# Optimization experiments

Hardware: AMD Instinct MI355X
Metric: run time of the kernel (lower is better)

The kernel has to match this reference:

```python
import jax, jax.numpy as jnp
import numpy as np

D_MODEL, N_HEAD, D_HEAD = 1024, 16, 64
QLEN, MLEN, BSZ = 1024, 512, 4
KLEN = QLEN + MLEN
RLEN = QLEN + KLEN
SCALE = 1.0 / (D_HEAD ** 0.5)
LN_EPS = 1e-12


def rel_shift(x, klen):
    # x: [i, j, b, n] -> shifted [i, klen, b, n]
    i, j, b, n = x.shape
    x = x.reshape(j, i, b, n)[1:].reshape(i, j - 1, b, n)
    return x[:, :klen]


def layer_norm(x, gamma, beta, eps=LN_EPS):
    mu = jnp.mean(x, axis=-1, keepdims=True)
    var = jnp.mean(jnp.square(x - mu), axis=-1, keepdims=True)
    return (x - mu) * jax.lax.rsqrt(var + eps) * gamma + beta


def setup_inputs() -> dict:
    key = jax.random.key(0)
    ks = jax.random.split(key, 16)
    std = 0.02
    h = jax.random.normal(ks[0], (QLEN, BSZ, D_MODEL), jnp.float32)
    r = jax.random.normal(ks[1], (RLEN, BSZ, D_MODEL), jnp.float32)
    mems = jax.random.normal(ks[2], (MLEN, BSZ, D_MODEL), jnp.float32)
    # binary float mask (1 = masked), broadcast over head dim
    attn_mask = (jax.random.uniform(ks[3], (QLEN, KLEN, BSZ, 1)) < 0.1).astype(jnp.float32)
    # one-hot segment matrix over 2 segment classes
    seg_ids = jax.random.randint(ks[4], (QLEN, KLEN, BSZ), 0, 2)
    seg_mat = jax.nn.one_hot(seg_ids, 2, dtype=jnp.float32)
    Wq = std * jax.random.normal(ks[5], (D_MODEL, N_HEAD, D_HEAD), jnp.float32)
    Wk = std * jax.random.normal(ks[6], (D_MODEL, N_HEAD, D_HEAD), jnp.float32)
    Wv = std * jax.random.normal(ks[7], (D_MODEL, N_HEAD, D_HEAD), jnp.float32)
    Wo = std * jax.random.normal(ks[8], (D_MODEL, N_HEAD, D_HEAD), jnp.float32)
    Wr = std * jax.random.normal(ks[9], (D_MODEL, N_HEAD, D_HEAD), jnp.float32)
    r_w_bias = jnp.zeros((N_HEAD, D_HEAD), jnp.float32)
    r_r_bias = jnp.zeros((N_HEAD, D_HEAD), jnp.float32)
    r_s_bias = jnp.zeros((N_HEAD, D_HEAD), jnp.float32)
    seg_embed = std * jax.random.normal(ks[10], (2, N_HEAD, D_HEAD), jnp.float32)
    ln_gamma = jnp.ones((D_MODEL,), jnp.float32)
    ln_beta = jnp.zeros((D_MODEL,), jnp.float32)
    return dict(h=h, r=r, mems=mems, attn_mask=attn_mask, seg_mat=seg_mat,
                Wq=Wq, Wk=Wk, Wv=Wv, Wo=Wo, Wr=Wr,
                r_w_bias=r_w_bias, r_r_bias=r_r_bias, r_s_bias=r_s_bias,
                seg_embed=seg_embed, ln_gamma=ln_gamma, ln_beta=ln_beta)


def reference(h, r, mems, attn_mask, seg_mat, Wq, Wk, Wv, Wo, Wr,
              r_w_bias, r_r_bias, r_s_bias, seg_embed, ln_gamma, ln_beta):
    cat = jnp.concatenate([mems, h], axis=0)  # [klen, b, d_model]
    q_head = jnp.einsum('ibh,hnd->ibnd', h, Wq)
    k_head_h = jnp.einsum('jbh,hnd->jbnd', cat, Wk)
    v_head_h = jnp.einsum('jbh,hnd->jbnd', cat, Wv)
    k_head_r = jnp.einsum('jbh,hnd->jbnd', r, Wr)

    klen = k_head_h.shape[0]
    ac = jnp.einsum('ibnd,jbnd->ijbn', q_head + r_w_bias, k_head_h)
    bd = jnp.einsum('ibnd,jbnd->ijbn', q_head + r_r_bias, k_head_r)
    bd = rel_shift(bd, klen)
    ef = jnp.einsum('ibnd,snd->ibns', q_head + r_s_bias, seg_embed)
    ef = jnp.einsum('ijbs,ibns->ijbn', seg_mat, ef)

    attn_score = (ac + bd + ef) * SCALE - 1e30 * attn_mask
    attn_prob = jax.nn.softmax(attn_score, axis=1)
    attn_vec = jnp.einsum('ijbn,jbnd->ibnd', attn_prob, v_head_h)

    attn_out = jnp.einsum('ibnd,hnd->ibh', attn_vec, Wo) + h  # residual
    return layer_norm(attn_out, ln_gamma, ln_beta)
```

## Files before the change

### kernel.cpp

```cpp
#include <hip/hip_runtime.h>

typedef unsigned short u16;
typedef __attribute__((ext_vector_type(8))) short bf16x8;
typedef __attribute__((ext_vector_type(4))) float f32x4;

constexpr int DM = 1024;
constexpr int NH = 16;
constexpr int DH = 64;
constexpr int QL = 1024;
constexpr int ML = 512;
constexpr int KL = 1536;
constexpr int RL = 2560;
constexpr int BS = 4;
constexpr int JT = KL / 64;
constexpr float SCALE = 0.125f;
constexpr float SC2 = 0.125f * 1.4426950408889634f;

static __device__ __forceinline__ u16 f2bf(float f) {
    unsigned u = __float_as_uint(f);
    u += 0x7fffu + ((u >> 16) & 1u);
    return (u16)(u >> 16);
}

static __device__ __forceinline__ void glds16(const u16* g, u16* l) {
    __builtin_amdgcn_global_load_lds(
        (const __attribute__((address_space(1))) unsigned int*)g,
        (__attribute__((address_space(3))) unsigned int*)l,
        16, 0, 0);
}

__global__ __launch_bounds__(256) void prep_kernel(
    const float* __restrict__ mems, const float* __restrict__ h,
    const float* __restrict__ r, const float* __restrict__ Wo,
    const float* __restrict__ mask, const float* __restrict__ segm,
    const float* __restrict__ Wq, const float* __restrict__ Wk,
    const float* __restrict__ Wv, const float* __restrict__ Wr,
    u16* __restrict__ catb, u16* __restrict__ rb, u16* __restrict__ wob,
    u16* __restrict__ WqT, u16* __restrict__ WkT,
    u16* __restrict__ WvT, u16* __restrict__ WrT,
    ulonglong2* __restrict__ pk)
{
    __shared__ float smem[64 * 65];
    const int id = blockIdx.x;
    const int t = threadIdx.x;

    if (id < 17408) {
        const long C0 = (long)ML * BS * DM;
        const long C1 = (long)KL * BS * DM;
        const long C2 = C1 + (long)RL * BS * DM;
        long g = ((long)id * 256 + t) * 4;
        const float* src; u16* dst;
        if (g < C0)      { src = mems + g;        dst = catb + g; }
        else if (g < C1) { src = h + (g - C0);    dst = catb + g; }
        else if (g < C2) { src = r + (g - C1);    dst = rb + (g - C1); }
        else             { src = Wo + (g - C2);   dst = wob + (g - C2); }
        float4 v = *(const float4*)src;
        unsigned lo = (unsigned)f2bf(v.x) | ((unsigned)f2bf(v.y) << 16);
        unsigned hi = (unsigned)f2bf(v.z) | ((unsigned)f2bf(v.w) << 16);
        *(uint2*)dst = make_uint2(lo, hi);
        return;
    }
    if (id < 18432) {
        float (*tile)[65] = (float(*)[65])smem;
        const int local = id - 17408;
        const float* W; u16* WT;
        switch (local >> 8) {
            case 0:  W = Wq; WT = WqT; break;
            case 1:  W = Wk; WT = WkT; break;
            case 2:  W = Wv; WT = WvT; break;
            default: W = Wr; WT = WrT; break;
        }
        const int k0 = (local & 15) * 64, n0 = ((local >> 4) & 15) * 64;
        const int tr = t >> 6, tc = t & 63;
        #pragma unroll
        for (int rr = 0; rr < 16; rr++) {
            int rw = tr + rr * 4;
            tile[rw][tc] = W[(size_t)(k0 + rw) * DM + n0 + tc];
        }
        __syncthreads();
        #pragma unroll
        for (int rr = 0; rr < 16; rr++) {
            int n = tr + rr * 4;
            WT[(size_t)(n0 + n) * DM + k0 + tc] = f2bf(tile[tc][n]);
        }
        return;
    }
    {
        float* mk = smem;
        float* sg = smem + 256;
        const int local = id - 18432;
        const int i = local / JT, jt = local - i * JT;
        const size_t base = ((size_t)i * KL + jt * 64) * BS;
        mk[t] = mask[base + t];
        float2 s2 = ((const float2*)(segm + base * 2))[t];
        sg[t] = s2.y;
        __syncthreads();
        const int b = t >> 6, lane = t & 63;
        const unsigned long long mb = __ballot(mk[lane * 4 + b] > 0.5f);
        const unsigned long long sb = __ballot(sg[lane * 4 + b] > 0.5f);
        if (lane == 0) {
            ulonglong2 v; v.x = mb; v.y = sb;
            pk[(((size_t)b * 16 + (i >> 6)) * JT + jt) * 64 + (i & 63)] = v;
        }
    }
}

__global__ __launch_bounds__(256) void proj_kernel(
    const u16* __restrict__ hb, const u16* __restrict__ catb,
    const u16* __restrict__ rb,
    const u16* __restrict__ WqT, const u16* __restrict__ WkT,
    const u16* __restrict__ WvT, const u16* __restrict__ WrT,
    float* __restrict__ q_s, u16* __restrict__ k_s,
    u16* __restrict__ v_s, u16* __restrict__ kr_s)
{
    __shared__ u16 a_lds[128][32];
    __shared__ u16 b_lds[128][32];
    const int id = blockIdx.x;
    const u16 *A, *B; void* C; int SEQ, MODE, local;
    if (id < 256)       { A = hb;   B = WqT; C = q_s;  SEQ = QL; MODE = 1; local = id; }
    else if (id < 640)  { A = catb; B = WkT; C = k_s;  SEQ = KL; MODE = 2; local = id - 256; }
    else if (id < 1024) { A = catb; B = WvT; C = v_s;  SEQ = KL; MODE = 2; local = id - 640; }
    else                { A = rb;   B = WrT; C = kr_s; SEQ = RL; MODE = 2; local = id - 1024; }
    const int bm = local >> 3, bnn = local & 7;

    const int t = threadIdx.x;
    const int w = t >> 6, lane = t & 63, l15 = lane & 15, q4 = lane >> 4;
    const int wm = (w >> 1) * 64, wn = (w & 1) * 64;
    const int srow = w * 32 + (lane >> 2);
    const int scol = (lane & 3) * 8;
    const u16* Ab = A + (size_t)(bm * 128 + srow) * DM + scol;
    const u16* Bb = B + (size_t)(bnn * 128 + srow) * DM + scol;
    u16* a_dst = &a_lds[w * 32][0];
    u16* b_dst = &b_lds[w * 32][0];

    f32x4 acc[4][4] = {};

    for (int k0 = 0; k0 < DM; k0 += 32) {
        __syncthreads();
        glds16(Ab + k0,           a_dst);
        glds16(Ab + k0 + 16 * DM, a_dst + 16 * 32);
        glds16(Bb + k0,           b_dst);
        glds16(Bb + k0 + 16 * DM, b_dst + 16 * 32);
        __syncthreads();
        bf16x8 af[4], bf[4];
        #pragma unroll
        for (int rt = 0; rt < 4; rt++)
            af[rt] = *(const bf16x8*)&a_lds[wm + rt * 16 + l15][q4 * 8];
        #pragma unroll
        for (int ct = 0; ct < 4; ct++)
            bf[ct] = *(const bf16x8*)&b_lds[wn + ct * 16 + l15][q4 * 8];
        #pragma unroll
        for (int rt = 0; rt < 4; rt++)
            #pragma unroll
            for (int ct = 0; ct < 4; ct++)
                acc[rt][ct] = __builtin_amdgcn_mfma_f32_16x16x32_bf16(
                    af[rt], bf[ct], acc[rt][ct], 0, 0, 0);
    }

    #pragma unroll
    for (int rt = 0; rt < 4; rt++)
      #pragma unroll
      for (int ct = 0; ct < 4; ct++)
        #pragma unroll
        for (int rg = 0; rg < 4; rg++) {
            const int R = bm * 128 + wm + rt * 16 + q4 * 4 + rg;
            const int Cc = bnn * 128 + wn + ct * 16 + l15;
            const float v = acc[rt][ct][rg];
            const int sq = R >> 2, bb = R & 3, hn = Cc >> 6, dd = Cc & 63;
            const size_t idx = ((size_t)(bb * NH + hn) * SEQ + sq) * DH + dd;
            if (MODE == 1) ((float*)C)[idx] = v;
            else           ((u16*)C)[idx]  = f2bf(v);
        }
}

__global__ __launch_bounds__(256) void vtrans_kernel(
    const u16* __restrict__ v_s, u16* __restrict__ vt_s)
{
    __shared__ u16 tl[64][72];
    const int j0 = blockIdx.x * 64;
    const int bn = blockIdx.y;
    const u16* vin = v_s + (size_t)bn * KL * DH;
    u16* vout = vt_s + (size_t)bn * DH * KL;
    const int t = threadIdx.x;
    const int r = t >> 3, c8 = (t & 7) * 8;
    #pragma unroll
    for (int it = 0; it < 64; it += 32)
        *(uint4*)&tl[r + it][c8] = *(const uint4*)(vin + (size_t)(j0 + r + it) * DH + c8);
    __syncthreads();
    #pragma unroll
    for (int it = 0; it < 64; it += 32) {
        const int d = r + it;
        u16 tmp[8];
        #pragma unroll
        for (int jj = 0; jj < 8; jj++) tmp[jj] = tl[c8 + jj][d];
        *(uint4*)&vout[(size_t)d * KL + j0 + c8] = *(const uint4*)tmp;
    }
}

__global__ __launch_bounds__(256) void ogemm_kernel(
    const u16* __restrict__ A, const u16* __restrict__ B,
    float* __restrict__ Cout)
{
    __shared__ u16 a_lds[128][32];
    __shared__ u16 b_lds[128][32];
    const int bm = blockIdx.x, bnn = blockIdx.y;
    const int t = threadIdx.x;
    const int w = t >> 6, lane = t & 63, l15 = lane & 15, q4 = lane >> 4;
    const int wm = (w >> 1) * 64, wn = (w & 1) * 64;
    const int srow = w * 32 + (lane >> 2);
    const int scol = (lane & 3) * 8;
    const u16* Ab = A + (size_t)(bm * 128 + srow) * DM + scol;
    const u16* Bb = B + (size_t)(bnn * 128 + srow) * DM + scol;
    u16* a_dst = &a_lds[w * 32][0];
    u16* b_dst = &b_lds[w * 32][0];

    f32x4 acc[4][4] = {};

    for (int k0 = 0; k0 < DM; k0 += 32) {
        __syncthreads();
        glds16(Ab + k0,           a_dst);
        glds16(Ab + k0 + 16 * DM, a_dst + 16 * 32);
        glds16(Bb + k0,           b_dst);
        glds16(Bb + k0 + 16 * DM, b_dst + 16 * 32);
        __syncthreads();
        bf16x8 af[4], bf[4];
        #pragma unroll
        for (int rt = 0; rt < 4; rt++)
            af[rt] = *(const bf16x8*)&a_lds[wm + rt * 16 + l15][q4 * 8];
        #pragma unroll
        for (int ct = 0; ct < 4; ct++)
            bf[ct] = *(const bf16x8*)&b_lds[wn + ct * 16 + l15][q4 * 8];
        #pragma unroll
        for (int rt = 0; rt < 4; rt++)
            #pragma unroll
            for (int ct = 0; ct < 4; ct++)
                acc[rt][ct] = __builtin_amdgcn_mfma_f32_16x16x32_bf16(
                    af[rt], bf[ct], acc[rt][ct], 0, 0, 0);
    }

    #pragma unroll
    for (int rt = 0; rt < 4; rt++)
      #pragma unroll
      for (int ct = 0; ct < 4; ct++)
        #pragma unroll
        for (int rg = 0; rg < 4; rg++) {
            const int R = bm * 128 + wm + rt * 16 + q4 * 4 + rg;
            const int C = bnn * 128 + wn + ct * 16 + l15;
            Cout[(size_t)R * DM + C] = acc[rt][ct][rg];
        }
}

#define FBAR() do { asm volatile("" ::: "memory");  \
                    __builtin_amdgcn_s_barrier();   \
                    asm volatile("" ::: "memory"); } while (0)

#define STAGE_K(TI)                                                            \
  {                                                                            \
    glds16(kg + (size_t)(TI) * 64 * DH,      &k2[(TI) & 1][0][w * 16][0]);     \
    glds16(kg + (size_t)(TI) * 64 * DH + 32, &k2[(TI) & 1][1][w * 16][0]);     \
  }

#define STAGE_V(TI)                                                            \
  {                                                                            \
    glds16(vg + (TI) * 64,      &v2[(TI) & 1][0][w * 16][0]);                  \
    glds16(vg + (TI) * 64 + 32, &v2[(TI) & 1][1][w * 16][0]);                  \
  }

#define STAGE_PK(TI)                                                           \
    glds16((const u16*)(pk_b + ((size_t)(TI) * 64 + lane)),                    \
           (u16*)&pk_lds[(TI) & 1][0]);

#define STAGE_KR(P)                                                            \
  {                                                                            \
    const int br_ = QL - i0 - 63 + (P) * 64 + w * 16 + krow;                   \
    glds16(kr_bn + (size_t)br_ * DH + ksrcseg * 8,       &krp[(P) & 3][w * 16][0]);     \
    glds16(kr_bn + (size_t)(br_ + 8) * DH + ksrcseg * 8, &krp[(P) & 3][w * 16 + 8][0]); \
  }

__global__ __launch_bounds__(256, 2) void attn_kernel(
    const float* __restrict__ q_s, const u16* __restrict__ k_s,
    const u16* __restrict__ vt_s, const u16* __restrict__ kr_s,
    const ulonglong2* __restrict__ pk,
    const float* __restrict__ rwb, const float* __restrict__ rrb,
    const float* __restrict__ rsb, const float* __restrict__ seg_embed,
    u16* __restrict__ av_s)
{
    __shared__ u16 k2[2][2][64][32];
    __shared__ u16 v2[2][2][64][32];
    __shared__ u16 krp[4][64][64];
    __shared__ u16 p_lds[4][16][64];
    __shared__ ulonglong2 pk_lds[2][64];
    __shared__ float e_lds[2][64];

    const int bn = blockIdx.x;
    const int itile = blockIdx.y;
    const int b = bn >> 4, n = bn & 15;
    const int t = threadIdx.x;
    const int w = t >> 6, lane = t & 63, l15 = lane & 15, q4 = lane >> 4;
    const int i0 = itile * 64;
    const int ib = i0 + w * 16;

    const float* q_bn = q_s + (size_t)bn * QL * DH;
    const u16* k_bn   = k_s  + (size_t)bn * KL * DH;
    const u16* vt_bn  = vt_s + (size_t)bn * DH * KL;
    const u16* kr_bn  = kr_s + (size_t)bn * RL * DH;
    const ulonglong2* pk_b = pk + ((size_t)b * 16 + itile) * JT * 64;

    if (t < 128) {
        const int rr = t >> 1, s = t & 1;
        const float* qrow = q_bn + (size_t)(i0 + rr) * DH;
        const float* se = seg_embed + (s * NH + n) * DH;
        const float* bias = rsb + n * DH;
        float acc = 0.f;
        #pragma unroll 16
        for (int d = 0; d < DH; d++) acc += (qrow[d] + bias[d]) * se[d];
        e_lds[s][rr] = acc * SC2;
    }

    bf16x8 qw[2], qr[2];
    {
        const float* qrow = q_bn + (size_t)(ib + l15) * DH;
        const float* bw = rwb + n * DH;
        const float* br = rrb + n * DH;
        #pragma unroll
        for (int kk = 0; kk < 2; kk++) {
            const int dbase = kk * 32 + q4 * 8;
            #pragma unroll
            for (int j = 0; j < 8; j++) {
                float qv = qrow[dbase + j];
                qw[kk][j] = (short)f2bf((qv + bw[dbase + j]) * SC2);
                qr[kk][j] = (short)f2bf((qv + br[dbase + j]) * SC2);
            }
        }
    }

    const int srow = lane >> 2;
    const int ssw  = ((lane & 3) ^ ((srow >> 1) & 3)) * 8;
    const u16* kg = k_bn  + (size_t)(w * 16 + srow) * DH + ssw;
    const u16* vg = vt_bn + (size_t)(w * 16 + srow) * KL + ssw;

    const int krow = lane >> 3;
    const int ksrcseg = (lane & 7) ^ krow;

    const int sA = ((q4)     ^ (l15 & 7)) * 8;
    const int sB = ((q4 + 4) ^ (l15 & 7)) * 8;
    const int ksw = (l15 >> 1) & 3;
    const int lrb_p = 48 - w * 16;

    f32x4 o[4] = {};
    float l_r[4] = {0.f, 0.f, 0.f, 0.f};

    STAGE_K(0); STAGE_V(0); STAGE_PK(0);
    STAGE_KR(0); STAGE_KR(1);
    STAGE_K(1); STAGE_V(1); STAGE_PK(1);
    STAGE_KR(2);
    asm volatile("s_waitcnt vmcnt(7) lgkmcnt(0)" ::: "memory");
    FBAR();

    float e_rg[2][4];
    #pragma unroll
    for (int rg = 0; rg < 4; rg++) {
        e_rg[0][rg] = e_lds[0][w * 16 + q4 * 4 + rg];
        e_rg[1][rg] = e_lds[1][w * 16 + q4 * 4 + rg];
    }

    #pragma unroll 1
    for (int jt = 0; jt < JT; jt++) {
        const int cb = jt & 1;

        __builtin_amdgcn_s_setprio(1);
        f32x4 sac[4] = {};
        #pragma unroll
        for (int ct = 0; ct < 4; ct++) {
            bf16x8 kb0 = *(const bf16x8*)&k2[cb][0][ct * 16 + l15][(q4 ^ ksw) * 8];
            bf16x8 kb1 = *(const bf16x8*)&k2[cb][1][ct * 16 + l15][(q4 ^ ksw) * 8];
            sac[ct] = __builtin_amdgcn_mfma_f32_16x16x32_bf16(qw[0], kb0, sac[ct], 0, 0, 0);
            sac[ct] = __builtin_amdgcn_mfma_f32_16x16x32_bf16(qw[1], kb1, sac[ct], 0, 0, 0);
        }

        f32x4 bacc[5] = {};
        #pragma unroll
        for (int wc = 0; wc < 5; wc++) {
            const int S = lrb_p + wc * 16;
            const u16* pr_ = &krp[(jt + (S >> 6)) & 3][(S & 63) + l15][0];
            bf16x8 b0 = *(const bf16x8*)(pr_ + sA);
            bf16x8 b1 = *(const bf16x8*)(pr_ + sB);
            bacc[wc] = __builtin_amdgcn_mfma_f32_16x16x32_bf16(qr[0], b0, bacc[wc], 0, 0, 0);
            bacc[wc] = __builtin_amdgcn_mfma_f32_16x16x32_bf16(qr[1], b1, bacc[wc], 0, 0, 0);
        }
        __builtin_amdgcn_s_setprio(0);

        #pragma unroll
        for (int rg = 0; rg < 4; rg++) {
            const int row = q4 * 4 + rg;
            const ulonglong2 mp = pk_lds[cb][w * 16 + row];
            const unsigned long long mx = mp.x >> l15;
            const unsigned long long sy = mp.y >> l15;
            const int v = l15 + 15 - row;
            const int srcl = (q4 << 4) | (v & 15);
            float sh[5];
            #pragma unroll
            for (int w5 = 0; w5 < 5; w5++)
                sh[w5] = __shfl(bacc[w5][rg], srcl, 64);
            const float e0 = e_rg[0][rg];
            const float e1 = e_rg[1][rg];
            float s0 = 0.f;
            #pragma unroll
            for (int ct = 0; ct < 4; ct++) {
                const float bd = (v < 16) ? sh[ct] : sh[ct + 1];
                const float ef = ((sy >> (ct * 16)) & 1ull) ? e1 : e0;
                float sarg = sac[ct][rg] + bd + ef;
                sarg = ((mx >> (ct * 16)) & 1ull) ? -1.0e30f : sarg;
                const float p = __builtin_amdgcn_exp2f(sarg);
                const int pg = (2 * ct + (l15 >> 3)) ^ (row & 7);
                p_lds[w][row][pg * 8 + (l15 & 7)] = f2bf(p);
                s0 += p;
            }
            l_r[rg] += s0;
        }

        __builtin_amdgcn_s_setprio(1);
        #pragma unroll
        for (int kk = 0; kk < 2; kk++) {
            const int pgr = ((kk * 4 + q4) ^ (l15 & 7)) * 8;
            bf16x8 pf = *(const bf16x8*)&p_lds[w][l15][pgr];
            #pragma unroll
            for (int dt = 0; dt < 4; dt++) {
                bf16x8 vf = *(const bf16x8*)&v2[cb][kk][dt * 16 + l15][(q4 ^ ksw) * 8];
                o[dt] = __builtin_amdgcn_mfma_f32_16x16x32_bf16(pf, vf, o[dt], 0, 0, 0);
            }
        }
        __builtin_amdgcn_s_setprio(0);

        if (jt < JT - 1) {
            FBAR();
            if (jt + 2 < JT) {
                STAGE_K(jt + 2);
                STAGE_V(jt + 2);
                STAGE_PK(jt + 2);
                STAGE_KR(jt + 3);
                asm volatile("s_waitcnt vmcnt(7)" ::: "memory");
            } else {
                asm volatile("s_waitcnt vmcnt(0)" ::: "memory");
            }
            FBAR();
        }
    }

    #pragma unroll
    for (int rg = 0; rg < 4; rg++) {
        #pragma unroll
        for (int off = 1; off < 16; off <<= 1)
            l_r[rg] += __shfl_xor(l_r[rg], off, 64);
        l_r[rg] = 1.f / l_r[rg];
    }
    #pragma unroll
    for (int dt = 0; dt < 4; dt++)
        #pragma unroll
        for (int rg = 0; rg < 4; rg++) {
            const int row = q4 * 4 + rg;
            const int ii = ib + row;
            const int d = dt * 16 + l15;
            const float v = o[dt][rg] * l_r[rg];
            av_s[(size_t)(ii * BS + b) * DM + n * DH + d] = f2bf(v);
        }
}

__global__ __launch_bounds__(256) void ln_kernel(
    const float* __restrict__ ao, const float* __restrict__ h,
    const float* __restrict__ gamma, const float* __restrict__ beta,
    float* __restrict__ out)
{
    __shared__ float red[8];
    const int row = blockIdx.x, t = threadIdx.x;
    const float* a  = ao + (size_t)row * DM;
    const float* hh = h  + (size_t)row * DM;
    float4 av = *(const float4*)(a + t * 4);
    float4 hv = *(const float4*)(hh + t * 4);
    const float x0 = av.x + hv.x, x1 = av.y + hv.y;
    const float x2 = av.z + hv.z, x3 = av.w + hv.w;
    float s = x0 + x1 + x2 + x3;
    float s2 = x0 * x0 + x1 * x1 + x2 * x2 + x3 * x3;
    #pragma unroll
    for (int off = 1; off < 64; off <<= 1) {
        s  += __shfl_xor(s, off, 64);
        s2 += __shfl_xor(s2, off, 64);
    }
    const int w = t >> 6;
    if ((t & 63) == 0) { red[w] = s; red[4 + w] = s2; }
    __syncthreads();
    s  = red[0] + red[1] + red[2] + red[3];
    s2 = red[4] + red[5] + red[6] + red[7];
    const float mu = s * (1.f / DM);
    const float var = s2 * (1.f / DM) - mu * mu;
    const float rstd = rsqrtf(var + 1e-12f);
    float4 g  = *(const float4*)(gamma + t * 4);
    float4 bb = *(const float4*)(beta + t * 4);
    float4 ov;
    ov.x = (x0 - mu) * rstd * g.x + bb.x;
    ov.y = (x1 - mu) * rstd * g.y + bb.y;
    ov.z = (x2 - mu) * rstd * g.z + bb.z;
    ov.w = (x3 - mu) * rstd * g.w + bb.w;
    *(float4*)(out + (size_t)row * DM + t * 4) = ov;
}

extern "C" void kernel_launch(void* const* d_in, const int* in_sizes, int n_in,
                              void* d_out, int out_size, void* d_ws, size_t ws_size,
                              hipStream_t stream) {
    (void)in_sizes; (void)n_in; (void)out_size; (void)ws_size;
    const float* h    = (const float*)d_in[0];
    const float* r    = (const float*)d_in[1];
    const float* mems = (const float*)d_in[2];
    const float* mask = (const float*)d_in[3];
    const float* segm = (const float*)d_in[4];
    const float* Wq   = (const float*)d_in[5];
    const float* Wk   = (const float*)d_in[6];
    const float* Wv   = (const float*)d_in[7];
    const float* Wo   = (const float*)d_in[8];
    const float* Wr   = (const float*)d_in[9];
    const float* rwb  = (const float*)d_in[10];
    const float* rrb  = (const float*)d_in[11];
    const float* rsb  = (const float*)d_in[12];
    const float* semb = (const float*)d_in[13];
    const float* gam  = (const float*)d_in[14];
    const float* bet  = (const float*)d_in[15];
    float* out = (float*)d_out;

    char* wsb = (char*)d_ws;
    size_t off = 0;
    auto alloc = [&](size_t bytes) -> void* {
        void* p = wsb + off; off += (bytes + 255) & ~(size_t)255; return p;
    };
    u16* catb = (u16*)alloc((size_t)KL * BS * DM * 2);
    u16* rb   = (u16*)alloc((size_t)RL * BS * DM * 2);
    u16* WqT  = (u16*)alloc((size_t)DM * DM * 2);
    u16* WkT  = (u16*)alloc((size_t)DM * DM * 2);
    u16* WvT  = (u16*)alloc((size_t)DM * DM * 2);
    u16* WrT  = (u16*)alloc((size_t)DM * DM * 2);
    u16* WoB  = (u16*)alloc((size_t)DM * DM * 2);
    float* q_s = (float*)alloc((size_t)BS * NH * QL * DH * 4);
    u16* k_s  = (u16*)alloc((size_t)BS * NH * KL * DH * 2);
    u16* vt_s = (u16*)alloc((size_t)BS * NH * KL * DH * 2);
    u16* kr_s = (u16*)alloc((size_t)BS * NH * RL * DH * 2 + 8192);
    u16* av_s = (u16*)alloc((size_t)QL * BS * DM * 2);
    float* ao_s = (float*)alloc((size_t)QL * BS * DM * 4);
    ulonglong2* pk = (ulonglong2*)alloc((size_t)BS * QL * JT * 16);
    u16* v_s = (u16*)ao_s;

    prep_kernel<<<43008, 256, 0, stream>>>(mems, h, r, Wo, mask, segm,
                                           Wq, Wk, Wv, Wr,
                                           catb, rb, WoB,
                                           WqT, WkT, WvT, WrT, pk);
    const u16* hb = catb + (size_t)2048 * DM;
    proj_kernel<<<1664, 256, 0, stream>>>(hb, catb, rb, WqT, WkT, WvT, WrT,
                                          q_s, k_s, v_s, kr_s);
    vtrans_kernel<<<dim3(JT, 64), 256, 0, stream>>>(v_s, vt_s);
    attn_kernel<<<dim3(64, 16), 256, 0, stream>>>(q_s, k_s, vt_s, kr_s, pk,
                                                  rwb, rrb, rsb, semb, av_s);
    ogemm_kernel<<<dim3(32, 8), 256, 0, stream>>>(av_s, WoB, ao_s);
    ln_kernel<<<4096, 256, 0, stream>>>(ao_s, h, gam, bet, out);
}
```

Baseline: 514.8 us.

## Double attention query tile to 128 rows and single-buffer V staging

Each attention block now handles 128 query rows instead of 64, with each wave owning two 16-row groups. Each K and V tile loaded into LDS is therefore reused across twice as many MFMAs, and the grid halves to 512 blocks. The packed mask/segment layout changes to match 128-row tiles. V staging drops to a single buffer loaded one iteration ahead and the KR prefetch moves to a mid-iteration barrier, which adds a barrier per loop, raises register pressure and cuts the number of blocks, possibly lowering occupancy on the CUs.

```diff
diff --git a/kernel.cpp b/kernel.cpp
--- a/kernel.cpp
+++ b/kernel.cpp
@@ -100,7 +100,7 @@
         const unsigned long long sb = __ballot(sg[lane * 4 + b] > 0.5f);
         if (lane == 0) {
             ulonglong2 v; v.x = mb; v.y = sb;
-            pk[(((size_t)b * 16 + (i >> 6)) * JT + jt) * 64 + (i & 63)] = v;
+            pk[(((size_t)b * 8 + (i >> 7)) * JT + jt) * 128 + (i & 127)] = v;
         }
     }
 }
@@ -262,17 +262,21 @@
 
 #define STAGE_V(TI)                                                            \
   {                                                                            \
-    glds16(vg + (TI) * 64,      &v2[(TI) & 1][0][w * 16][0]);                  \
-    glds16(vg + (TI) * 64 + 32, &v2[(TI) & 1][1][w * 16][0]);                  \
+    glds16(vg + (TI) * 64,      &v1[0][w * 16][0]);                            \
+    glds16(vg + (TI) * 64 + 32, &v1[1][w * 16][0]);                            \
   }
 
 #define STAGE_PK(TI)                                                           \
-    glds16((const u16*)(pk_b + ((size_t)(TI) * 64 + lane)),                    \
-           (u16*)&pk_lds[(TI) & 1][0]);
+  {                                                                            \
+    glds16((const u16*)(pk_b + ((size_t)(TI) * 128 + lane)),                   \
+           (u16*)&pk_lds[(TI) & 1][0]);                                        \
+    glds16((const u16*)(pk_b + ((size_t)(TI) * 128 + 64 + lane)),              \
+           (u16*)&pk_lds[(TI) & 1][64]);                                       \
+  }
 
 #define STAGE_KR(P)                                                            \
   {                                                                            \
-    const int br_ = QL - i0 - 63 + (P) * 64 + w * 16 + krow;                   \
+    const int br_ = PbaseG + (P) * 64 + w * 16 + krow;                         \
     glds16(kr_bn + (size_t)br_ * DH + ksrcseg * 8,       &krp[(P) & 3][w * 16][0]);     \
     glds16(kr_bn + (size_t)(br_ + 8) * DH + ksrcseg * 8, &krp[(P) & 3][w * 16 + 8][0]); \
   }
@@ -286,27 +290,28 @@
     u16* __restrict__ av_s)
 {
     __shared__ u16 k2[2][2][64][32];
-    __shared__ u16 v2[2][2][64][32];
+    __shared__ u16 v1[2][64][32];
     __shared__ u16 krp[4][64][64];
-    __shared__ u16 p_lds[4][16][64];
-    __shared__ ulonglong2 pk_lds[2][64];
-    __shared__ float e_lds[2][64];
+    __shared__ u16 p_lds[4][32][64];
+    __shared__ ulonglong2 pk_lds[2][128];
+    __shared__ float e_lds[2][128];
 
     const int bn = blockIdx.x;
     const int itile = blockIdx.y;
     const int b = bn >> 4, n = bn & 15;
     const int t = threadIdx.x;
     const int w = t >> 6, lane = t & 63, l15 = lane & 15, q4 = lane >> 4;
-    const int i0 = itile * 64;
-    const int ib = i0 + w * 16;
+    const int i0 = itile * 128;
+    const int ib = i0 + w * 32;
+    const int PbaseG = QL - i0 - 127;
 
     const float* q_bn = q_s + (size_t)bn * QL * DH;
     const u16* k_bn   = k_s  + (size_t)bn * KL * DH;
     const u16* vt_bn  = vt_s + (size_t)bn * DH * KL;
     const u16* kr_bn  = kr_s + (size_t)bn * RL * DH;
-    const ulonglong2* pk_b = pk + ((size_t)b * 16 + itile) * JT * 64;
-
-    if (t < 128) {
+    const ulonglong2* pk_b = pk + ((size_t)b * 8 + itile) * (JT * 128);
+
+    {
         const int rr = t >> 1, s = t & 1;
         const float* qrow = q_bn + (size_t)(i0 + rr) * DH;
         const float* se = seg_embed + (s * NH + n) * DH;
@@ -317,9 +322,10 @@
         e_lds[s][rr] = acc * SC2;
     }
 
-    bf16x8 qw[2], qr[2];
-    {
-        const float* qrow = q_bn + (size_t)(ib + l15) * DH;
+    bf16x8 qw[2][2], qr[2][2];
+    #pragma unroll
+    for (int g = 0; g < 2; g++) {
+        const float* qrow = q_bn + (size_t)(ib + g * 16 + l15) * DH;
         const float* bw = rwb + n * DH;
         const float* br = rrb + n * DH;
         #pragma unroll
@@ -328,8 +334,8 @@
             #pragma unroll
             for (int j = 0; j < 8; j++) {
                 float qv = qrow[dbase + j];
-                qw[kk][j] = (short)f2bf((qv + bw[dbase + j]) * SC2);
-                qr[kk][j] = (short)f2bf((qv + br[dbase + j]) * SC2);
+                qw[g][kk][j] = (short)f2bf((qv + bw[dbase + j]) * SC2);
+                qr[g][kk][j] = (short)f2bf((qv + br[dbase + j]) * SC2);
             }
         }
     }
@@ -345,125 +351,146 @@
     const int sA = ((q4)     ^ (l15 & 7)) * 8;
     const int sB = ((q4 + 4) ^ (l15 & 7)) * 8;
     const int ksw = (l15 >> 1) & 3;
-    const int lrb_p = 48 - w * 16;
-
-    f32x4 o[4] = {};
-    float l_r[4] = {0.f, 0.f, 0.f, 0.f};
-
-    STAGE_K(0); STAGE_V(0); STAGE_PK(0);
-    STAGE_KR(0); STAGE_KR(1);
-    STAGE_K(1); STAGE_V(1); STAGE_PK(1);
-    STAGE_KR(2);
-    asm volatile("s_waitcnt vmcnt(7) lgkmcnt(0)" ::: "memory");
+
+    f32x4 o[2][4] = {};
+    float l_r[2][4] = {};
+
+    STAGE_K(0); STAGE_PK(0);
+    STAGE_KR(0); STAGE_KR(1); STAGE_KR(2);
+    STAGE_V(0); STAGE_K(1); STAGE_PK(1);
+    asm volatile("s_waitcnt vmcnt(6) lgkmcnt(0)" ::: "memory");
     FBAR();
 
-    float e_rg[2][4];
-    #pragma unroll
-    for (int rg = 0; rg < 4; rg++) {
-        e_rg[0][rg] = e_lds[0][w * 16 + q4 * 4 + rg];
-        e_rg[1][rg] = e_lds[1][w * 16 + q4 * 4 + rg];
-    }
+    float e_rg[2][2][4];
+    #pragma unroll
+    for (int g = 0; g < 2; g++)
+        #pragma unroll
+        for (int rg = 0; rg < 4; rg++) {
+            e_rg[0][g][rg] = e_lds[0][w * 32 + g * 16 + q4 * 4 + rg];
+            e_rg[1][g][rg] = e_lds[1][w * 32 + g * 16 + q4 * 4 + rg];
+        }
 
     #pragma unroll 1
     for (int jt = 0; jt < JT; jt++) {
         const int cb = jt & 1;
 
         __builtin_amdgcn_s_setprio(1);
-        f32x4 sac[4] = {};
+        f32x4 sac[2][4] = {};
         #pragma unroll
         for (int ct = 0; ct < 4; ct++) {
             bf16x8 kb0 = *(const bf16x8*)&k2[cb][0][ct * 16 + l15][(q4 ^ ksw) * 8];
             bf16x8 kb1 = *(const bf16x8*)&k2[cb][1][ct * 16 + l15][(q4 ^ ksw) * 8];
-            sac[ct] = __builtin_amdgcn_mfma_f32_16x16x32_bf16(qw[0], kb0, sac[ct], 0, 0, 0);
-            sac[ct] = __builtin_amdgcn_mfma_f32_16x16x32_bf16(qw[1], kb1, sac[ct], 0, 0, 0);
-        }
-
-        f32x4 bacc[5] = {};
-        #pragma unroll
-        for (int wc = 0; wc < 5; wc++) {
-            const int S = lrb_p + wc * 16;
-            const u16* pr_ = &krp[(jt + (S >> 6)) & 3][(S & 63) + l15][0];
-            bf16x8 b0 = *(const bf16x8*)(pr_ + sA);
-            bf16x8 b1 = *(const bf16x8*)(pr_ + sB);
-            bacc[wc] = __builtin_amdgcn_mfma_f32_16x16x32_bf16(qr[0], b0, bacc[wc], 0, 0, 0);
-            bacc[wc] = __builtin_amdgcn_mfma_f32_16x16x32_bf16(qr[1], b1, bacc[wc], 0, 0, 0);
+            sac[0][ct] = __builtin_amdgcn_mfma_f32_16x16x32_bf16(qw[0][0], kb0, sac[0][ct], 0, 0, 0);
+            sac[0][ct] = __builtin_amdgcn_mfma_f32_16x16x32_bf16(qw[0][1], kb1, sac[0][ct], 0, 0, 0);
+            sac[1][ct] = __builtin_amdgcn_mfma_f32_16x16x32_bf16(qw[1][0], kb0, sac[1][ct], 0, 0, 0);
+            sac[1][ct] = __builtin_amdgcn_mfma_f32_16x16x32_bf16(qw[1][1], kb1, sac[1][ct], 0, 0, 0);
         }
         __builtin_amdgcn_s_setprio(0);
 
         #pragma unroll
-        for (int rg = 0; rg < 4; rg++) {
-            const int row = q4 * 4 + rg;
-            const ulonglong2 mp = pk_lds[cb][w * 16 + row];
-            const unsigned long long mx = mp.x >> l15;
-            const unsigned long long sy = mp.y >> l15;
-            const int v = l15 + 15 - row;
-            const int srcl = (q4 << 4) | (v & 15);
-            float sh[5];
-            #pragma unroll
-            for (int w5 = 0; w5 < 5; w5++)
-                sh[w5] = __shfl(bacc[w5][rg], srcl, 64);
-            const float e0 = e_rg[0][rg];
-            const float e1 = e_rg[1][rg];
-            float s0 = 0.f;
-            #pragma unroll
-            for (int ct = 0; ct < 4; ct++) {
-                const float bd = (v < 16) ? sh[ct] : sh[ct + 1];
-                const float ef = ((sy >> (ct * 16)) & 1ull) ? e1 : e0;
-                float sarg = sac[ct][rg] + bd + ef;
-                sarg = ((mx >> (ct * 16)) & 1ull) ? -1.0e30f : sarg;
-                const float p = __builtin_amdgcn_exp2f(sarg);
-                const int pg = (2 * ct + (l15 >> 3)) ^ (row & 7);
-                p_lds[w][row][pg * 8 + (l15 & 7)] = f2bf(p);
-                s0 += p;
+        for (int g = 0; g < 2; g++) {
+            const int bg = 112 - w * 32 - g * 16;
+            __builtin_amdgcn_s_setprio(1);
+            f32x4 bacc[5] = {};
+            #pragma unroll
+            for (int wc = 0; wc < 5; wc++) {
+                const int S = bg + wc * 16;
+                const u16* pr_ = &krp[(jt + (S >> 6)) & 3][(S & 63) + l15][0];
+                bf16x8 b0 = *(const bf16x8*)(pr_ + sA);
+                bf16x8 b1 = *(const bf16x8*)(pr_ + sB);
+                bacc[wc] = __builtin_amdgcn_mfma_f32_16x16x32_bf16(qr[g][0], b0, bacc[wc], 0, 0, 0);
+                bacc[wc] = __builtin_amdgcn_mfma_f32_16x16x32_bf16(qr[g][1], b1, bacc[wc], 0, 0, 0);
             }
-            l_r[rg] += s0;
-        }
+            __builtin_amdgcn_s_setprio(0);
+
+            #pragma unroll
+            for (int rg = 0; rg < 4; rg++) {
+                const int row = q4 * 4 + rg;
+                const ulonglong2 mp = pk_lds[cb][w * 32 + g * 16 + row];
+                const unsigned long long mx = mp.x >> l15;
+                const unsigned long long sy = mp.y >> l15;
+                const int v = l15 + 15 - row;
+                const int srcl = (q4 << 4) | (v & 15);
+                float sh[5];
+                #pragma unroll
+                for (int w5 = 0; w5 < 5; w5++)
+                    sh[w5] = __shfl(bacc[w5][rg], srcl, 64);
+                const float e0 = e_rg[0][g][rg];
+                const float e1 = e_rg[1][g][rg];
+                float s0 = 0.f;
+                #pragma unroll
+                for (int ct = 0; ct < 4; ct++) {
+                    const float bd = (v < 16) ? sh[ct] : sh[ct + 1];
+                    const float ef = ((sy >> (ct * 16)) & 1ull) ? e1 : e0;
+                    float sarg = sac[g][ct][rg] + bd + ef;
+                    sarg = ((mx >> (ct * 16)) & 1ull) ? -1.0e30f : sarg;
+                    const float p = __builtin_amdgcn_exp2f(sarg);
+                    const int pg = (2 * ct + (l15 >> 3)) ^ (row & 7);
+                    p_lds[w][g * 16 + row][pg * 8 + (l15 & 7)] = f2bf(p);
+                    s0 += p;
+                }
+                l_r[g][rg] += s0;
+            }
+        }
+
+        if (jt == JT - 1) asm volatile("s_waitcnt vmcnt(0)" ::: "memory");
+        else              asm volatile("s_waitcnt vmcnt(4)" ::: "memory");
+        FBAR();
+        if (jt < JT - 1) STAGE_KR(jt + 3);
 
         __builtin_amdgcn_s_setprio(1);
         #pragma unroll
         for (int kk = 0; kk < 2; kk++) {
-            const int pgr = ((kk * 4 + q4) ^ (l15 & 7)) * 8;
-            bf16x8 pf = *(const bf16x8*)&p_lds[w][l15][pgr];
-            #pragma unroll
-            for (int dt = 0; dt < 4; dt++) {
-                bf16x8 vf = *(const bf16x8*)&v2[cb][kk][dt * 16 + l15][(q4 ^ ksw) * 8];
-                o[dt] = __builtin_amdgcn_mfma_f32_16x16x32_bf16(pf, vf, o[dt], 0, 0, 0);
+            bf16x8 vf[4];
+            #pragma unroll
+            for (int dt = 0; dt < 4; dt++)
+                vf[dt] = *(const bf16x8*)&v1[kk][dt * 16 + l15][(q4 ^ ksw) * 8];
+            #pragma unroll
+            for (int g = 0; g < 2; g++) {
+                const int pgr = ((kk * 4 + q4) ^ (l15 & 7)) * 8;
+                bf16x8 pf = *(const bf16x8*)&p_lds[w][g * 16 + l15][pgr];
+                #pragma unroll
+                for (int dt = 0; dt < 4; dt++)
+                    o[g][dt] = __builtin_amdgcn_mfma_f32_16x16x32_bf16(pf, vf[dt], o[g][dt], 0, 0, 0);
             }
         }
         __builtin_amdgcn_s_setprio(0);
 
         if (jt < JT - 1) {
             FBAR();
+            STAGE_V(jt + 1);
             if (jt + 2 < JT) {
                 STAGE_K(jt + 2);
-                STAGE_V(jt + 2);
                 STAGE_PK(jt + 2);
-                STAGE_KR(jt + 3);
-                asm volatile("s_waitcnt vmcnt(7)" ::: "memory");
+                asm volatile("s_waitcnt vmcnt(6)" ::: "memory");
             } else {
-                asm volatile("s_waitcnt vmcnt(0)" ::: "memory");
+                asm volatile("s_waitcnt vmcnt(2)" ::: "memory");
             }
             FBAR();
         }
     }
 
     #pragma unroll
-    for (int rg = 0; rg < 4; rg++) {
-        #pragma unroll
-        for (int off = 1; off < 16; off <<= 1)
-            l_r[rg] += __shfl_xor(l_r[rg], off, 64);
-        l_r[rg] = 1.f / l_r[rg];
-    }
-    #pragma unroll
-    for (int dt = 0; dt < 4; dt++)
+    for (int g = 0; g < 2; g++)
         #pragma unroll
         for (int rg = 0; rg < 4; rg++) {
-            const int row = q4 * 4 + rg;
-            const int ii = ib + row;
-            const int d = dt * 16 + l15;
-            const float v = o[dt][rg] * l_r[rg];
-            av_s[(size_t)(ii * BS + b) * DM + n * DH + d] = f2bf(v);
-        }
+            #pragma unroll
+            for (int off = 1; off < 16; off <<= 1)
+                l_r[g][rg] += __shfl_xor(l_r[g][rg], off, 64);
+            l_r[g][rg] = 1.f / l_r[g][rg];
+        }
+    #pragma unroll
+    for (int g = 0; g < 2; g++)
+        #pragma unroll
+        for (int dt = 0; dt < 4; dt++)
+            #pragma unroll
+            for (int rg = 0; rg < 4; rg++) {
+                const int row = q4 * 4 + rg;
+                const int ii = ib + g * 16 + row;
+                const int d = dt * 16 + l15;
+                const float v = o[g][dt][rg] * l_r[g][rg];
+                av_s[(size_t)(ii * BS + b) * DM + n * DH + d] = f2bf(v);
+            }
 }
 
 __global__ __launch_bounds__(256) void ln_kernel(
@@ -555,8 +582,8 @@
     proj_kernel<<<1664, 256, 0, stream>>>(hb, catb, rb, WqT, WkT, WvT, WrT,
                                           q_s, k_s, v_s, kr_s);
     vtrans_kernel<<<dim3(JT, 64), 256, 0, stream>>>(v_s, vt_s);
-    attn_kernel<<<dim3(64, 16), 256, 0, stream>>>(q_s, k_s, vt_s, kr_s, pk,
-                                                  rwb, rrb, rsb, semb, av_s);
+    attn_kernel<<<dim3(64, 8), 256, 0, stream>>>(q_s, k_s, vt_s, kr_s, pk,
+                                                 rwb, rrb, rsb, semb, av_s);
     ogemm_kernel<<<dim3(32, 8), 256, 0, stream>>>(av_s, WoB, ao_s);
     ln_kernel<<<4096, 256, 0, stream>>>(ao_s, h, gam, bet, out);
 }
```

After: 480.3 us. 6.7% less time.

## Double attention query tile to 128 rows with 8 waves sharing K/V/Kr tiles

Applied to the files above, without the earlier changes.

The attention kernel now processes 128 query rows per block with 512 threads (8 waves), halving the grid and letting each staged K, V and relative-key tile serve twice as many queries. Staging is split so each wave issues one load per tile. V drops to a single buffer and Kr gets a deeper 4-slot prefetch with an extra barrier mid-iteration. The packed mask layout is changed to 128-row tiles to match, and the segment bias is read from LDS per row instead of held in registers. Fewer blocks and an added per-iteration barrier may reduce latency hiding, and the launch-bounds occupancy target is raised.

```diff
diff --git a/kernel.cpp b/kernel.cpp
--- a/kernel.cpp
+++ b/kernel.cpp
@@ -100,7 +100,7 @@
         const unsigned long long sb = __ballot(sg[lane * 4 + b] > 0.5f);
         if (lane == 0) {
             ulonglong2 v; v.x = mb; v.y = sb;
-            pk[(((size_t)b * 16 + (i >> 6)) * JT + jt) * 64 + (i & 63)] = v;
+            pk[(((size_t)b * 8 + (i >> 7)) * JT + jt) * 128 + (i & 127)] = v;
         }
     }
 }
@@ -255,29 +255,21 @@
                     asm volatile("" ::: "memory"); } while (0)
 
 #define STAGE_K(TI)                                                            \
-  {                                                                            \
-    glds16(kg + (size_t)(TI) * 64 * DH,      &k2[(TI) & 1][0][w * 16][0]);     \
-    glds16(kg + (size_t)(TI) * 64 * DH + 32, &k2[(TI) & 1][1][w * 16][0]);     \
-  }
+    glds16(kg + (size_t)(TI) * 64 * DH, &k2[(TI) & 1][w >> 2][(w & 3) * 16][0])
 
 #define STAGE_V(TI)                                                            \
-  {                                                                            \
-    glds16(vg + (TI) * 64,      &v2[(TI) & 1][0][w * 16][0]);                  \
-    glds16(vg + (TI) * 64 + 32, &v2[(TI) & 1][1][w * 16][0]);                  \
-  }
+    glds16(vg + (size_t)(TI) * 64, &v1[w >> 2][(w & 3) * 16][0])
 
 #define STAGE_PK(TI)                                                           \
-    glds16((const u16*)(pk_b + ((size_t)(TI) * 64 + lane)),                    \
-           (u16*)&pk_lds[(TI) & 1][0]);
+    { if (w < 2)                                                               \
+        glds16((const u16*)(pk_b + ((size_t)(TI) * 128 + w * 64 + lane)),      \
+               (u16*)&pk_lds[(TI) & 1][w * 64]); }
 
 #define STAGE_KR(P)                                                            \
-  {                                                                            \
-    const int br_ = QL - i0 - 63 + (P) * 64 + w * 16 + krow;                   \
-    glds16(kr_bn + (size_t)br_ * DH + ksrcseg * 8,       &krp[(P) & 3][w * 16][0]);     \
-    glds16(kr_bn + (size_t)(br_ + 8) * DH + ksrcseg * 8, &krp[(P) & 3][w * 16 + 8][0]); \
-  }
-
-__global__ __launch_bounds__(256, 2) void attn_kernel(
+    glds16(kr_bn + (size_t)(PbaseG + (P) * 64 + w * 8 + krow8) * DH + kseg8 * 8, \
+           &krp[(P) & 3][w * 8][0])
+
+__global__ __launch_bounds__(512, 4) void attn_kernel(
     const float* __restrict__ q_s, const u16* __restrict__ k_s,
     const u16* __restrict__ vt_s, const u16* __restrict__ kr_s,
     const ulonglong2* __restrict__ pk,
@@ -286,27 +278,28 @@
     u16* __restrict__ av_s)
 {
     __shared__ u16 k2[2][2][64][32];
-    __shared__ u16 v2[2][2][64][32];
+    __shared__ u16 v1[2][64][32];
     __shared__ u16 krp[4][64][64];
-    __shared__ u16 p_lds[4][16][64];
-    __shared__ ulonglong2 pk_lds[2][64];
-    __shared__ float e_lds[2][64];
+    __shared__ u16 p_lds[8][16][64];
+    __shared__ ulonglong2 pk_lds[2][128];
+    __shared__ float e_lds[128][2];
 
     const int bn = blockIdx.x;
     const int itile = blockIdx.y;
     const int b = bn >> 4, n = bn & 15;
     const int t = threadIdx.x;
     const int w = t >> 6, lane = t & 63, l15 = lane & 15, q4 = lane >> 4;
-    const int i0 = itile * 64;
+    const int i0 = itile * 128;
     const int ib = i0 + w * 16;
+    const int PbaseG = QL - i0 - 127;
 
     const float* q_bn = q_s + (size_t)bn * QL * DH;
     const u16* k_bn   = k_s  + (size_t)bn * KL * DH;
     const u16* vt_bn  = vt_s + (size_t)bn * DH * KL;
     const u16* kr_bn  = kr_s + (size_t)bn * RL * DH;
-    const ulonglong2* pk_b = pk + ((size_t)b * 16 + itile) * JT * 64;
-
-    if (t < 128) {
+    const ulonglong2* pk_b = pk + ((size_t)b * 8 + itile) * (JT * 128);
+
+    if (t < 256) {
         const int rr = t >> 1, s = t & 1;
         const float* qrow = q_bn + (size_t)(i0 + rr) * DH;
         const float* se = seg_embed + (s * NH + n) * DH;
@@ -314,7 +307,7 @@
         float acc = 0.f;
         #pragma unroll 16
         for (int d = 0; d < DH; d++) acc += (qrow[d] + bias[d]) * se[d];
-        e_lds[s][rr] = acc * SC2;
+        e_lds[rr][s] = acc * SC2;
     }
 
     bf16x8 qw[2], qr[2];
@@ -336,33 +329,26 @@
 
     const int srow = lane >> 2;
     const int ssw  = ((lane & 3) ^ ((srow >> 1) & 3)) * 8;
-    const u16* kg = k_bn  + (size_t)(w * 16 + srow) * DH + ssw;
-    const u16* vg = vt_bn + (size_t)(w * 16 + srow) * KL + ssw;
-
-    const int krow = lane >> 3;
-    const int ksrcseg = (lane & 7) ^ krow;
+    const u16* kg = k_bn  + (size_t)((w & 3) * 16 + srow) * DH + (w >> 2) * 32 + ssw;
+    const u16* vg = vt_bn + (size_t)((w & 3) * 16 + srow) * KL + (w >> 2) * 32 + ssw;
+
+    const int krow8 = lane >> 3;
+    const int kseg8 = (lane & 7) ^ krow8;
 
     const int sA = ((q4)     ^ (l15 & 7)) * 8;
     const int sB = ((q4 + 4) ^ (l15 & 7)) * 8;
     const int ksw = (l15 >> 1) & 3;
-    const int lrb_p = 48 - w * 16;
+    const int bg = 112 - w * 16;
 
     f32x4 o[4] = {};
     float l_r[4] = {0.f, 0.f, 0.f, 0.f};
 
-    STAGE_K(0); STAGE_V(0); STAGE_PK(0);
-    STAGE_KR(0); STAGE_KR(1);
-    STAGE_K(1); STAGE_V(1); STAGE_PK(1);
-    STAGE_KR(2);
-    asm volatile("s_waitcnt vmcnt(7) lgkmcnt(0)" ::: "memory");
+    STAGE_K(0); STAGE_PK(0);
+    STAGE_KR(0); STAGE_KR(1); STAGE_KR(2);
+    STAGE_KR(3); STAGE_V(0); STAGE_K(1); STAGE_PK(1);
+    if (w < 2) asm volatile("s_waitcnt vmcnt(4) lgkmcnt(0)" ::: "memory");
+    else       asm volatile("s_waitcnt vmcnt(3) lgkmcnt(0)" ::: "memory");
     FBAR();
-
-    float e_rg[2][4];
-    #pragma unroll
-    for (int rg = 0; rg < 4; rg++) {
-        e_rg[0][rg] = e_lds[0][w * 16 + q4 * 4 + rg];
-        e_rg[1][rg] = e_lds[1][w * 16 + q4 * 4 + rg];
-    }
 
     #pragma unroll 1
     for (int jt = 0; jt < JT; jt++) {
@@ -381,7 +367,7 @@
         f32x4 bacc[5] = {};
         #pragma unroll
         for (int wc = 0; wc < 5; wc++) {
-            const int S = lrb_p + wc * 16;
+            const int S = bg + wc * 16;
             const u16* pr_ = &krp[(jt + (S >> 6)) & 3][(S & 63) + l15][0];
             bf16x8 b0 = *(const bf16x8*)(pr_ + sA);
             bf16x8 b1 = *(const bf16x8*)(pr_ + sB);
@@ -402,13 +388,12 @@
             #pragma unroll
             for (int w5 = 0; w5 < 5; w5++)
                 sh[w5] = __shfl(bacc[w5][rg], srcl, 64);
-            const float e0 = e_rg[0][rg];
-            const float e1 = e_rg[1][rg];
+            const float2 e2 = *(const float2*)&e_lds[w * 16 + row][0];
             float s0 = 0.f;
             #pragma unroll
             for (int ct = 0; ct < 4; ct++) {
                 const float bd = (v < 16) ? sh[ct] : sh[ct + 1];
-                const float ef = ((sy >> (ct * 16)) & 1ull) ? e1 : e0;
+                const float ef = ((sy >> (ct * 16)) & 1ull) ? e2.y : e2.x;
                 float sarg = sac[ct][rg] + bd + ef;
                 sarg = ((mx >> (ct * 16)) & 1ull) ? -1.0e30f : sarg;
                 const float p = __builtin_amdgcn_exp2f(sarg);
@@ -419,6 +404,15 @@
             l_r[rg] += s0;
         }
 
+        if (jt + 4 < JT) {
+            if (w < 2) asm volatile("s_waitcnt vmcnt(2)" ::: "memory");
+            else       asm volatile("s_waitcnt vmcnt(1)" ::: "memory");
+        } else {
+            asm volatile("s_waitcnt vmcnt(0)" ::: "memory");
+        }
+        FBAR();
+        if (jt + 4 < JT) STAGE_KR(jt + 4);
+
         __builtin_amdgcn_s_setprio(1);
         #pragma unroll
         for (int kk = 0; kk < 2; kk++) {
@@ -426,7 +420,7 @@
             bf16x8 pf = *(const bf16x8*)&p_lds[w][l15][pgr];
             #pragma unroll
             for (int dt = 0; dt < 4; dt++) {
-                bf16x8 vf = *(const bf16x8*)&v2[cb][kk][dt * 16 + l15][(q4 ^ ksw) * 8];
+                bf16x8 vf = *(const bf16x8*)&v1[kk][dt * 16 + l15][(q4 ^ ksw) * 8];
                 o[dt] = __builtin_amdgcn_mfma_f32_16x16x32_bf16(pf, vf, o[dt], 0, 0, 0);
             }
         }
@@ -434,12 +428,11 @@
 
         if (jt < JT - 1) {
             FBAR();
-            if (jt + 2 < JT) {
-                STAGE_K(jt + 2);
-                STAGE_V(jt + 2);
-                STAGE_PK(jt + 2);
-                STAGE_KR(jt + 3);
-                asm volatile("s_waitcnt vmcnt(7)" ::: "memory");
+            STAGE_V(jt + 1);
+            if (jt + 2 < JT) { STAGE_K(jt + 2); STAGE_PK(jt + 2); }
+            if (jt + 4 < JT) {
+                if (w < 2) asm volatile("s_waitcnt vmcnt(4)" ::: "memory");
+                else       asm volatile("s_waitcnt vmcnt(3)" ::: "memory");
             } else {
                 asm volatile("s_waitcnt vmcnt(0)" ::: "memory");
             }
@@ -555,8 +548,8 @@
     proj_kernel<<<1664, 256, 0, stream>>>(hb, catb, rb, WqT, WkT, WvT, WrT,
                                           q_s, k_s, v_s, kr_s);
     vtrans_kernel<<<dim3(JT, 64), 256, 0, stream>>>(v_s, vt_s);
-    attn_kernel<<<dim3(64, 16), 256, 0, stream>>>(q_s, k_s, vt_s, kr_s, pk,
-                                                  rwb, rrb, rsb, semb, av_s);
+    attn_kernel<<<dim3(64, 8), 512, 0, stream>>>(q_s, k_s, vt_s, kr_s, pk,
+                                                 rwb, rrb, rsb, semb, av_s);
     ogemm_kernel<<<dim3(32, 8), 256, 0, stream>>>(av_s, WoB, ao_s);
     ln_kernel<<<4096, 256, 0, stream>>>(ao_s, h, gam, bet, out);
 }
```

New measurement: 526.6 us. 2.3% more time.
